# Optimization experiments

Measured on AMD Instinct MI355X. Metric: run time of the kernel, lower is better.

Reference implementation:

```python
import jax, jax.numpy as jnp
import numpy as np

H, W = 2000, 1000  # T_out buffer: (1, 2000, 1000); conv spatial grid matches
FILL = -9999.0


def _winit(k, o, c):
    return jax.random.normal(k, (o, c), jnp.float32) * (1.0 / np.sqrt(c))


def setup_inputs() -> dict:
    key = jax.random.key(0)
    ks = jax.random.split(key, 6)
    inp = jax.random.normal(ks[0], (1, 9, H, W), dtype=jnp.float32)
    T_out = jnp.zeros((1, H, W), dtype=jnp.float32)
    flat = jnp.arange(H * W, dtype=jnp.int32)
    T_indices = jnp.stack([flat // W, flat % W]).reshape(2, H, W)
    return {
        "input": inp,
        "T_out": T_out,
        "T_indices": T_indices,
        "w1": _winit(ks[1], 18, 9), "b1": jnp.zeros((18,), jnp.float32),
        "w2": _winit(ks[2], 36, 18), "b2": jnp.zeros((36,), jnp.float32),
        "w3": _winit(ks[3], 36, 36), "b3": jnp.zeros((36,), jnp.float32),
        "w4": _winit(ks[4], 1, 36), "b4": jnp.zeros((1,), jnp.float32),
    }


def _conv1x1(x, w, b):
    # 1x1 conv == channel matmul: x (b,c,h,w), w (o,c)
    return jnp.einsum('bchw,oc->bohw', x, w) + b[None, :, None, None]


def reference(input, T_out, T_indices, w1, b1, w2, b2, w3, b3, w4, b4):
    x = jax.nn.relu(_conv1x1(input, w1, b1))
    x = jax.nn.relu(_conv1x1(x, w2, b2))
    x = jax.nn.relu(_conv1x1(x, w3, b3))
    x = _conv1x1(x, w4, b4)  # (1,1,H,W)
    # fill buffer with -9999 then indexed scatter of the fused scores
    T = jnp.full(T_out.shape, FILL, dtype=T_out.dtype)
    T = T.at[:, T_indices[0], T_indices[1]].set(x[0, 0])
    # MaxPool2d([1,1000]) -> max over W; MaxPool2d([2000,1]) -> max over H
    out1 = T.max(axis=2).squeeze()  # (2000,)
    out2 = T.max(axis=1).squeeze()  # (1000,)
    return (out1, out2)
```

## Files before the change

kernel.cpp:

```cpp
#include <hip/hip_runtime.h>

typedef _Float16 f16x8 __attribute__((ext_vector_type(8)));
typedef _Float16 f16x4 __attribute__((ext_vector_type(4)));
typedef __fp16 h16x2 __attribute__((ext_vector_type(2)));
typedef float f32x4 __attribute__((ext_vector_type(4)));

#define HH 2000
#define WW 1000
#define HWSZ (HH * WW)
#define NEG_INF (-3.0e38f)

__device__ __forceinline__ unsigned fenc(float f) {
    unsigned u = __float_as_uint(f);
    return (u & 0x80000000u) ? ~u : (u | 0x80000000u);
}
__device__ __forceinline__ float fdec(unsigned k) {
    unsigned u = (k & 0x80000000u) ? (k & 0x7fffffffu) : ~k;
    return __uint_as_float(u);
}

__global__ void decode_buckets(unsigned* __restrict__ buck, int n) {
    int i = blockIdx.x * blockDim.x + threadIdx.x;
    if (i < n) {
        unsigned k = buck[i];
        ((float*)buck)[i] = fdec(k);
    }
}


__global__ __launch_bounds__(128) void mlp_max_mfma(
    const float* __restrict__ in,
    const float* __restrict__ w1, const float* __restrict__ b1,
    const float* __restrict__ w2, const float* __restrict__ b2,
    const float* __restrict__ w3, const float* __restrict__ b3,
    const float* __restrict__ w4, const float* __restrict__ b4,
    unsigned* __restrict__ rowbuck, unsigned* __restrict__ colbuck) {
    __shared__ _Float16 lds[2][2 * 1280];
    __shared__ float rowsm[2][16][16];

    const int tx = threadIdx.x;
    const int wv = threadIdx.y;
    const int px = tx & 15;
    const int q = tx >> 4;

    _Float16* s0buf1 = &lds[wv][0];
    _Float16* s0buf2 = &lds[wv][640];
    _Float16* s1buf1 = &lds[wv][1280];
    _Float16* s1buf2 = &lds[wv][1920];

    f16x8 A1[2], A2[3], A3s0[3], A3s1[3];
#pragma unroll
    for (int t = 0; t < 2; ++t) {
        const int m = t * 16 + px;
#pragma unroll
        for (int j = 0; j < 8; ++j) {
            const int k = q * 8 + j;
            float v = 0.f;
            if (m < 18) {
                if (k < 9) v = w1[m * 9 + k];
                else if (k == 9) v = b1[m];
            }
            A1[t][j] = (_Float16)v;
        }
    }
#pragma unroll
    for (int t = 0; t < 3; ++t) {
        const int m = t * 16 + px;
#pragma unroll
        for (int j = 0; j < 8; ++j) {
            const int k = q * 8 + j;
            float v = 0.f;
            if (m < 36) {
                if (k < 18) v = w2[m * 18 + k];
                else if (k == 18) v = b2[m];
            }
            A2[t][j] = (_Float16)v;
        }
    }
#pragma unroll
    for (int t = 0; t < 3; ++t) {
        const int m = t * 16 + px;
#pragma unroll
        for (int j = 0; j < 8; ++j) {
            const int k = q * 8 + j;
            float v = 0.f;
            if (m < 36 && k < 32) v = w3[m * 36 + k];
            A3s0[t][j] = (_Float16)v;
            float v2 = 0.f;
            const int k2 = 32 + k;
            if (m < 36) {
                if (k2 < 36) v2 = w3[m * 36 + k2];
                else if (k2 == 36) v2 = b3[m];
            }
            A3s1[t][j] = (_Float16)v2;
        }
    }

    float w4r[3][4];
#pragma unroll
    for (int t = 0; t < 3; ++t)
#pragma unroll
        for (int rg = 0; rg < 4; ++rg) {
            const int ch = t * 16 + q * 4 + rg;
            w4r[t][rg] = (ch < 36) ? w4[ch] : 0.f;
        }
    const float b4s = b4[0];

    const int col = blockIdx.x * 32 + wv * 16 + px;
    const int colc = (col < WW) ? col : (WW - 1);
    const bool colok = (col < WW);
    const int rb = blockIdx.y * 16;

    float colmax = NEG_INF;
    const f32x4 zf4 = {0.f, 0.f, 0.f, 0.f};
    const h16x2 z2 = {(__fp16)0.f, (__fp16)0.f};

    union U8 { f16x8 v; h16x2 h[4]; };
    union U4 { f16x4 v; h16x2 h[2]; };

    int off[8];
#pragma unroll
    for (int j = 0; j < 8; ++j) {
        const int c = q * 8 + j;
        off[j] = (c < 9) ? (c * HWSZ + colc) : 0;
    }

    float b0a[8], b0b[8], b1a[8], b1b[8], b2a[8], b2b[8], b3a[8], b3b[8];

    auto LOAD = [&](int r, float (&v0)[8], float (&v1)[8]) {
        const float* rbase = in + (size_t)r * WW;
#pragma unroll
        for (int j = 0; j < 8; ++j) {
            const int c = q * 8 + j;
            float x0 = (c == 9) ? 1.f : 0.f;
            float x1 = x0;
            if (c < 9) {
                x0 = rbase[off[j]];
                x1 = rbase[off[j] + WW];
            }
            v0[j] = x0;
            v1[j] = x1;
        }
    };

    auto COMPUTE = [&](int it, const float (&v0)[8], const float (&v1)[8]) {
        U8 b0u, b1u;
#pragma unroll
        for (int j = 0; j < 4; ++j) {
            b0u.h[j] = __builtin_amdgcn_cvt_pkrtz(v0[2 * j], v0[2 * j + 1]);
            b1u.h[j] = __builtin_amdgcn_cvt_pkrtz(v1[2 * j], v1[2 * j + 1]);
        }
        const f16x8 bin0 = b0u.v;
        const f16x8 bin1 = b1u.v;

        f32x4 D1a[2], D1b[2];
#pragma unroll
        for (int t = 0; t < 2; ++t) {
            D1a[t] = __builtin_amdgcn_mfma_f32_16x16x32_f16(A1[t], bin0, zf4, 0, 0, 0);
            D1b[t] = __builtin_amdgcn_mfma_f32_16x16x32_f16(A1[t], bin1, zf4, 0, 0, 0);
        }
#pragma unroll
        for (int t = 0; t < 2; ++t) {
            U4 h0, h1;
            h0.h[0] = __builtin_elementwise_max(
                __builtin_amdgcn_cvt_pkrtz(D1a[t][0], D1a[t][1]), z2);
            h0.h[1] = __builtin_elementwise_max(
                __builtin_amdgcn_cvt_pkrtz(D1a[t][2], D1a[t][3]), z2);
            h1.h[0] = __builtin_elementwise_max(
                __builtin_amdgcn_cvt_pkrtz(D1b[t][0], D1b[t][1]), z2);
            h1.h[1] = __builtin_elementwise_max(
                __builtin_amdgcn_cvt_pkrtz(D1b[t][2], D1b[t][3]), z2);
            if (t == 1 && q == 0) {
                h0.v[2] = (_Float16)1.f;
                h1.v[2] = (_Float16)1.f;
            }
            *(f16x4*)&s0buf1[px * 40 + t * 16 + q * 4] = h0.v;
            *(f16x4*)&s1buf1[px * 40 + t * 16 + q * 4] = h1.v;
        }
        const f16x8 B2a = *(const f16x8*)&s0buf1[px * 40 + q * 8];
        const f16x8 B2b = *(const f16x8*)&s1buf1[px * 40 + q * 8];

        f32x4 D2a[3], D2b[3];
#pragma unroll
        for (int t = 0; t < 3; ++t) {
            D2a[t] = __builtin_amdgcn_mfma_f32_16x16x32_f16(A2[t], B2a, zf4, 0, 0, 0);
            D2b[t] = __builtin_amdgcn_mfma_f32_16x16x32_f16(A2[t], B2b, zf4, 0, 0, 0);
        }
#pragma unroll
        for (int t = 0; t < 3; ++t) {
            U4 h0, h1;
            h0.h[0] = __builtin_elementwise_max(
                __builtin_amdgcn_cvt_pkrtz(D2a[t][0], D2a[t][1]), z2);
            h0.h[1] = __builtin_elementwise_max(
                __builtin_amdgcn_cvt_pkrtz(D2a[t][2], D2a[t][3]), z2);
            h1.h[0] = __builtin_elementwise_max(
                __builtin_amdgcn_cvt_pkrtz(D2b[t][0], D2b[t][1]), z2);
            h1.h[1] = __builtin_elementwise_max(
                __builtin_amdgcn_cvt_pkrtz(D2b[t][2], D2b[t][3]), z2);
            if (t < 2) {
                *(f16x4*)&s0buf2[px * 40 + t * 16 + q * 4] = h0.v;
                *(f16x4*)&s1buf2[px * 40 + t * 16 + q * 4] = h1.v;
            } else if (q == 0) {
                *(f16x4*)&s0buf2[px * 40 + 32] = h0.v;
                *(f16x4*)&s1buf2[px * 40 + 32] = h1.v;
            }
        }
        const f16x8 B3a0 = *(const f16x8*)&s0buf2[px * 40 + q * 8];
        const f16x8 B3b0 = *(const f16x8*)&s1buf2[px * 40 + q * 8];
        f16x8 B3a1 = {0, 0, 0, 0, 0, 0, 0, 0};
        f16x8 B3b1 = {0, 0, 0, 0, 0, 0, 0, 0};
        if (q == 0) {
            const f16x4 t0 = *(const f16x4*)&s0buf2[px * 40 + 32];
            const f16x4 t1 = *(const f16x4*)&s1buf2[px * 40 + 32];
#pragma unroll
            for (int j = 0; j < 4; ++j) { B3a1[j] = t0[j]; B3b1[j] = t1[j]; }
            B3a1[4] = (_Float16)1.f;
            B3b1[4] = (_Float16)1.f;
        }

        f32x4 D3a[3], D3b[3];
#pragma unroll
        for (int t = 0; t < 3; ++t) {
            D3a[t] = __builtin_amdgcn_mfma_f32_16x16x32_f16(A3s0[t], B3a0, zf4, 0, 0, 0);
            D3a[t] = __builtin_amdgcn_mfma_f32_16x16x32_f16(A3s1[t], B3a1, D3a[t], 0, 0, 0);
            D3b[t] = __builtin_amdgcn_mfma_f32_16x16x32_f16(A3s0[t], B3b0, zf4, 0, 0, 0);
            D3b[t] = __builtin_amdgcn_mfma_f32_16x16x32_f16(A3s1[t], B3b1, D3b[t], 0, 0, 0);
        }

        float sa = 0.f, sb = 0.f;
#pragma unroll
        for (int t = 0; t < 3; ++t)
#pragma unroll
            for (int rg = 0; rg < 4; ++rg) {
                sa = fmaf(w4r[t][rg], fmaxf(D3a[t][rg], 0.f), sa);
                sb = fmaf(w4r[t][rg], fmaxf(D3b[t][rg], 0.f), sb);
            }
        sa += __shfl_xor(sa, 16, 64); sb += __shfl_xor(sb, 16, 64);
        sa += __shfl_xor(sa, 32, 64); sb += __shfl_xor(sb, 32, 64);
        sa += b4s; sb += b4s;

        sa = colok ? sa : NEG_INF;
        sb = colok ? sb : NEG_INF;
        colmax = fmaxf(colmax, fmaxf(sa, sb));

        if (q == 0) rowsm[wv][it * 2][px] = sa;
        else if (q == 1) rowsm[wv][it * 2 + 1][px] = sb;
    };

    LOAD(rb + 0, b0a, b0b);
    LOAD(rb + 2, b1a, b1b);
#pragma unroll 1
    for (int it = 0; it < 8; it += 4) {
        LOAD(rb + (it + 2) * 2, b2a, b2b);
        COMPUTE(it, b0a, b0b);
        LOAD(rb + (it + 3) * 2, b3a, b3b);
        COMPUTE(it + 1, b1a, b1b);
        if (it == 0) LOAD(rb + (it + 4) * 2, b0a, b0b);
        COMPUTE(it + 2, b2a, b2b);
        if (it == 0) LOAD(rb + (it + 5) * 2, b1a, b1b);
        COMPUTE(it + 3, b3a, b3b);
    }

    if (q == 0 && colok) atomicMax(&colbuck[col], fenc(colmax));
    if (tx < 16) {
        const f32x4 v0 = *(const f32x4*)&rowsm[wv][tx][0];
        const f32x4 v1 = *(const f32x4*)&rowsm[wv][tx][4];
        const f32x4 v2 = *(const f32x4*)&rowsm[wv][tx][8];
        const f32x4 v3 = *(const f32x4*)&rowsm[wv][tx][12];
        float m = NEG_INF;
#pragma unroll
        for (int j = 0; j < 4; ++j) {
            m = fmaxf(m, fmaxf(fmaxf(v0[j], v1[j]), fmaxf(v2[j], v3[j])));
        }
        atomicMax(&rowbuck[rb + tx], fenc(m));
    }
}

extern "C" void kernel_launch(void* const* d_in, const int* in_sizes, int n_in,
                              void* d_out, int out_size, void* d_ws, size_t ws_size,
                              hipStream_t stream) {
    const float* in = (const float*)d_in[0];
    const float* w1 = (const float*)d_in[3];
    const float* b1 = (const float*)d_in[4];
    const float* w2 = (const float*)d_in[5];
    const float* b2 = (const float*)d_in[6];
    const float* w3 = (const float*)d_in[7];
    const float* b3 = (const float*)d_in[8];
    const float* w4 = (const float*)d_in[9];
    const float* b4 = (const float*)d_in[10];

    unsigned* buck = (unsigned*)d_out;

    (void)hipMemsetAsync(buck, 0, 3000 * sizeof(unsigned), stream);

    dim3 block(64, 2);
    dim3 grid(32, 125);
    mlp_max_mfma<<<grid, block, 0, stream>>>(in, w1, b1, w2, b2, w3, b3, w4, b4,
                                             buck, buck + 2000);

    decode_buckets<<<(3000 + 255) / 256, 256, 0, stream>>>(buck, 3000);
}
```

Baseline: 204.6 us.

## Enlarge per-block row tile to 40 with double-buffered loads and split FMA chains

Each block now covers 40 rows instead of 16, so the grid shrinks from 125 to 50 row-blocks. This amortizes weight-fragment setup and per-block row/column atomics over more work. The four-deep load pipeline becomes a two-buffer ping-pong, which frees registers but leaves less loads in flight. The final 36-wide dot product is split into four independent FMA chains to shorten the dependency chain. The trade-off is fewer blocks, so less parallelism to hide memory latency.

```diff
diff --git a/kernel.cpp b/kernel.cpp
--- a/kernel.cpp
+++ b/kernel.cpp
@@ -9,6 +9,7 @@
 #define WW 1000
 #define HWSZ (HH * WW)
 #define NEG_INF (-3.0e38f)
+#define RT 40
 
 __device__ __forceinline__ unsigned fenc(float f) {
     unsigned u = __float_as_uint(f);
@@ -35,18 +36,18 @@
     const float* __restrict__ w3, const float* __restrict__ b3,
     const float* __restrict__ w4, const float* __restrict__ b4,
     unsigned* __restrict__ rowbuck, unsigned* __restrict__ colbuck) {
-    __shared__ _Float16 lds[2][2 * 1280];
-    __shared__ float rowsm[2][16][16];
+    __shared__ _Float16 albuf[2][2 * 1280];
+    __shared__ float rowsm[2][RT][16];
 
     const int tx = threadIdx.x;
     const int wv = threadIdx.y;
     const int px = tx & 15;
     const int q = tx >> 4;
 
-    _Float16* s0buf1 = &lds[wv][0];
-    _Float16* s0buf2 = &lds[wv][640];
-    _Float16* s1buf1 = &lds[wv][1280];
-    _Float16* s1buf2 = &lds[wv][1920];
+    _Float16* s0buf1 = &albuf[wv][0];
+    _Float16* s0buf2 = &albuf[wv][640];
+    _Float16* s1buf1 = &albuf[wv][1280];
+    _Float16* s1buf2 = &albuf[wv][1920];
 
     f16x8 A1[2], A2[3], A3s0[3], A3s1[3];
 #pragma unroll
@@ -109,7 +110,7 @@
     const int col = blockIdx.x * 32 + wv * 16 + px;
     const int colc = (col < WW) ? col : (WW - 1);
     const bool colok = (col < WW);
-    const int rb = blockIdx.y * 16;
+    const int rb = blockIdx.y * RT;
 
     float colmax = NEG_INF;
     const f32x4 zf4 = {0.f, 0.f, 0.f, 0.f};
@@ -125,7 +126,7 @@
         off[j] = (c < 9) ? (c * HWSZ + colc) : 0;
     }
 
-    float b0a[8], b0b[8], b1a[8], b1b[8], b2a[8], b2b[8], b3a[8], b3b[8];
+    float ca[8], cb[8], na[8], nb[8];
 
     auto LOAD = [&](int r, float (&v0)[8], float (&v1)[8]) {
         const float* rbase = in + (size_t)r * WW;
@@ -227,14 +228,21 @@
             D3b[t] = __builtin_amdgcn_mfma_f32_16x16x32_f16(A3s1[t], B3b1, D3b[t], 0, 0, 0);
         }
 
-        float sa = 0.f, sb = 0.f;
-#pragma unroll
-        for (int t = 0; t < 3; ++t)
-#pragma unroll
-            for (int rg = 0; rg < 4; ++rg) {
-                sa = fmaf(w4r[t][rg], fmaxf(D3a[t][rg], 0.f), sa);
-                sb = fmaf(w4r[t][rg], fmaxf(D3b[t][rg], 0.f), sb);
-            }
+        float sa0 = 0.f, sa1 = 0.f, sa2 = 0.f, sa3 = 0.f;
+        float sb0 = 0.f, sb1 = 0.f, sb2 = 0.f, sb3 = 0.f;
+#pragma unroll
+        for (int t = 0; t < 3; ++t) {
+            sa0 = fmaf(w4r[t][0], fmaxf(D3a[t][0], 0.f), sa0);
+            sa1 = fmaf(w4r[t][1], fmaxf(D3a[t][1], 0.f), sa1);
+            sa2 = fmaf(w4r[t][2], fmaxf(D3a[t][2], 0.f), sa2);
+            sa3 = fmaf(w4r[t][3], fmaxf(D3a[t][3], 0.f), sa3);
+            sb0 = fmaf(w4r[t][0], fmaxf(D3b[t][0], 0.f), sb0);
+            sb1 = fmaf(w4r[t][1], fmaxf(D3b[t][1], 0.f), sb1);
+            sb2 = fmaf(w4r[t][2], fmaxf(D3b[t][2], 0.f), sb2);
+            sb3 = fmaf(w4r[t][3], fmaxf(D3b[t][3], 0.f), sb3);
+        }
+        float sa = (sa0 + sa1) + (sa2 + sa3);
+        float sb = (sb0 + sb1) + (sb2 + sb3);
         sa += __shfl_xor(sa, 16, 64); sb += __shfl_xor(sb, 16, 64);
         sa += __shfl_xor(sa, 32, 64); sb += __shfl_xor(sb, 32, 64);
         sa += b4s; sb += b4s;
@@ -247,22 +255,17 @@
         else if (q == 1) rowsm[wv][it * 2 + 1][px] = sb;
     };
 
-    LOAD(rb + 0, b0a, b0b);
-    LOAD(rb + 2, b1a, b1b);
+    LOAD(rb, ca, cb);
 #pragma unroll 1
-    for (int it = 0; it < 8; it += 4) {
-        LOAD(rb + (it + 2) * 2, b2a, b2b);
-        COMPUTE(it, b0a, b0b);
-        LOAD(rb + (it + 3) * 2, b3a, b3b);
-        COMPUTE(it + 1, b1a, b1b);
-        if (it == 0) LOAD(rb + (it + 4) * 2, b0a, b0b);
-        COMPUTE(it + 2, b2a, b2b);
-        if (it == 0) LOAD(rb + (it + 5) * 2, b1a, b1b);
-        COMPUTE(it + 3, b3a, b3b);
+    for (int it = 0; it < RT / 2; it += 2) {
+        LOAD(rb + (it + 1) * 2, na, nb);
+        COMPUTE(it, ca, cb);
+        if (it < RT / 2 - 2) LOAD(rb + (it + 2) * 2, ca, cb);
+        COMPUTE(it + 1, na, nb);
     }
 
     if (q == 0 && colok) atomicMax(&colbuck[col], fenc(colmax));
-    if (tx < 16) {
+    if (tx < RT) {
         const f32x4 v0 = *(const f32x4*)&rowsm[wv][tx][0];
         const f32x4 v1 = *(const f32x4*)&rowsm[wv][tx][4];
         const f32x4 v2 = *(const f32x4*)&rowsm[wv][tx][8];
@@ -294,7 +297,7 @@
     (void)hipMemsetAsync(buck, 0, 3000 * sizeof(unsigned), stream);
 
     dim3 block(64, 2);
-    dim3 grid(32, 125);
+    dim3 grid(32, 50);
     mlp_max_mfma<<<grid, block, 0, stream>>>(in, w1, b1, w2, b2, w3, b3, w4, b4,
                                              buck, buck + 2000);
 
```

After: 190.7 us. -6.8%, faster.
